# Kernel tuning notes

Measured on AMD Instinct MI355X. Metric: run time of the kernel, lower is better.

## Reference

```python
import jax, jax.numpy as jnp
import numpy as np

B, L = 64, 262144
KERNEL_SIZES = [65, 33, 17, 9]
K_LIST = [L // ks for ks in KERNEL_SIZES]  # sparsity_density per kernel


def conv1d_same(x, w):
    # x: [B, 1, L], w: [kernel_size] -> torch F.conv1d(..., padding='same')
    return jax.lax.conv_general_dilated(
        x, w[None, None, :], window_strides=(1,), padding='SAME',
        dimension_numbers=('NCH', 'OIH', 'NCH'))


def topk_absolutes_1d(x, k):
    # keep the k largest-|x| entries along the last axis, zero elsewhere
    _, idx = jax.lax.top_k(jnp.abs(x), k)          # [B, 1, k]
    kept = jnp.take_along_axis(x, idx, axis=-1)    # [B, 1, k]
    b = jnp.arange(x.shape[0])[:, None, None]
    c = jnp.arange(x.shape[1])[None, :, None]
    return jnp.zeros_like(x).at[b, c, idx].set(kept)


def setup_inputs() -> dict:
    key = jax.random.key(0)
    batch_x = jax.random.normal(key, (B, 1, L), dtype=jnp.float32)
    inp = {'batch_x': batch_x}
    for i, ks in enumerate(KERNEL_SIZES):
        inp[f'w{i}'] = 0.1 * jnp.ones((ks,), dtype=jnp.float32)
    return inp


def reference(batch_x, w0, w1, w2, w3):
    weights = [w0, w1, w2, w3]
    recon_sum = jnp.zeros_like(batch_x)
    for w, k in zip(weights, K_LIST):
        similarity = conv1d_same(batch_x, w)
        activations = topk_absolutes_1d(similarity, k)
        recon_sum = recon_sum + conv1d_same(activations, w)
    return recon_sum
```

## Files before the change

kernel.cpp:

```cpp
#include <hip/hip_runtime.h>
#include <stdint.h>


#define B_ 64
#define L_ 262144
#define NBINS 8192
#define CAPC 8192
#define LCAP 1024
#define TSUB 2304
#define SUBS 8
#define NCHUNK 15
#define XSTG 2560
#define T5 2304
#define NT5 114
#define NSCAN 16

typedef unsigned int u32;

__device__ const int d_K[4] = {4032, 7943, 15420, 29127};

__device__ __forceinline__ void k1_stage(const float* __restrict__ xr, int base,
                                         float* dst, int tid)
{
  const bool interior = (base >= 32) && (base - 32 + XSTG <= L_);
  if (interior) {
    const float* g0 = xr + (base - 32);
    const int wv = tid >> 6, lane = tid & 63;
#pragma unroll
    for (int r = 0; r < 3; ++r) {
      const int off = (r * 4 + wv) * 256;
      if (off < XSTG) {
        __builtin_amdgcn_global_load_lds(
            (const __attribute__((address_space(1))) unsigned int*)(const void*)(g0 + off + lane * 4),
            (__attribute__((address_space(3))) unsigned int*)(void*)(dst + off),
            16, 0, 0);
      }
    }
  } else {
    for (int i = tid; i < TSUB + 64; i += 256) {
      const int g = base - 32 + i;
      dst[i] = (g >= 0 && g < L_) ? xr[g] : 0.0f;
    }
  }
}

template<int KS>
__device__ __forceinline__ void k1_body(
    const float* __restrict__ xr, const float* __restrict__ w,
    float* __restrict__ yrow,
    float* xb0, float* xb1, float* yb0, float* yb1)
{
  constexpr int PAD = KS / 2;
  constexpr int OFF = 32 - PAD;
  const int tid = threadIdx.x;

  float wreg[KS];
#pragma unroll
  for (int j = 0; j < KS; ++j) wreg[j] = w[j];

  const int base0 = blockIdx.x * SUBS * TSUB;
  k1_stage(xr, base0, xb0, tid);
  __syncthreads();

  int pendBase = -1;
  float* pendBuf = nullptr;

  for (int it = 0; it < SUBS; ++it) {
    const int base = base0 + it * TSUB;
    if (base >= L_) break;
    float* xcur = (it & 1) ? xb1 : xb0;
    float* xnxt = (it & 1) ? xb0 : xb1;
    float* ycur = (it & 1) ? yb1 : yb0;
    const int nbase = base + TSUB;
    if (it + 1 < SUBS && nbase < L_)
      k1_stage(xr, nbase, xnxt, tid);

    if (pendBase >= 0) {
      const int n4 = min(TSUB, L_ - pendBase) >> 2;
      float4* dst = (float4*)(yrow + pendBase);
      for (int i = tid; i < n4; i += 256) dst[i] = ((const float4*)pendBuf)[i];
    }

    float acc[9];
#pragma unroll
    for (int r = 0; r < 9; ++r) acc[r] = 0.0f;
    const int q0 = tid * 9;
#pragma unroll
    for (int p = 0; p < KS + 8; ++p) {
      float xv = xcur[q0 + OFF + p];
#pragma unroll
      for (int r = 0; r < 9; ++r) {
        const int j = p - r;
        if (j >= 0 && j < KS) acc[r] = fmaf(xv, wreg[j], acc[r]);
      }
    }

#pragma unroll
    for (int r = 0; r < 9; ++r) ycur[q0 + r] = acc[r];
    pendBase = base; pendBuf = ycur;
    __syncthreads();
  }

  if (pendBase >= 0) {
    const int n4 = min(TSUB, L_ - pendBase) >> 2;
    float4* dst = (float4*)(yrow + pendBase);
    for (int i = tid; i < n4; i += 256) dst[i] = ((const float4*)pendBuf)[i];
  }
}

__global__ __launch_bounds__(256) void k1_conv(
    const float* __restrict__ x, const float* __restrict__ w0,
    const float* __restrict__ w1, const float* __restrict__ w2,
    const float* __restrict__ w3, float* __restrict__ y,
    int kk0, int ng)
{
  __shared__ __align__(16) float xb[2][XSTG];
  __shared__ __align__(16) float yb[2][TSUB];
  const int kg = blockIdx.y;
  const int row = blockIdx.z;
  const int rkl = row * ng + kg;
  const int kk = kk0 + kg;
  const float* xr = x + (size_t)row * L_;
  float* yrow = y + (size_t)rkl * L_;
  switch (kk) {
    case 0:  k1_body<65>(xr, w0, yrow, xb[0], xb[1], yb[0], yb[1]); break;
    case 1:  k1_body<33>(xr, w1, yrow, xb[0], xb[1], yb[0], yb[1]); break;
    case 2:  k1_body<17>(xr, w2, yrow, xb[0], xb[1], yb[0], yb[1]); break;
    default: k1_body< 9>(xr, w3, yrow, xb[0], xb[1], yb[0], yb[1]); break;
  }
}

__global__ __launch_bounds__(256) void k2_hist(
    const float* __restrict__ y, u32* __restrict__ ghist, int ng)
{
  __shared__ u32 h32[NBINS / 2];
  const int tid = threadIdx.x;
  const int rkl = blockIdx.z * ng + blockIdx.y;
  for (int i = tid; i < NBINS / 2; i += 256) h32[i] = 0u;
  __syncthreads();
  const float* yr = y + (size_t)rkl * L_;
  const int c0 = blockIdx.x * (L_ / NSCAN);
  const float4* src = (const float4*)(yr + c0);
  for (int i = tid; i < (L_ / NSCAN) / 4; i += 256) {
    float4 v = src[i];
    const float* vf = (const float*)&v;
#pragma unroll
    for (int c = 0; c < 4; ++c) {
      u32 bin = (__float_as_uint(vf[c]) & 0x7fffffffu) >> 18;
      atomicAdd(&h32[bin >> 1], 1u << (16 * (bin & 1)));
    }
  }
  __syncthreads();
  u32* gh = ghist + (size_t)rkl * NBINS;
  for (int i = tid; i < NBINS / 2; i += 256) {
    u32 v = h32[i];
    u32 lo = v & 0xffffu, hi = v >> 16;
    if (lo) atomicAdd(&gh[2 * i], lo);
    if (hi) atomicAdd(&gh[2 * i + 1], hi);
  }
}

__global__ __launch_bounds__(256) void k2_findbin(
    const u32* __restrict__ ghist, u32* __restrict__ bbin, u32* __restrict__ rrem,
    int kk0, int ng)
{
  __shared__ u32 h[NBINS];
  __shared__ u32 ssum[256];
  const int rkl = blockIdx.x;
  const u32 k = (u32)d_K[kk0 + (rkl % ng)];
  const u32* gh = ghist + (size_t)rkl * NBINS;
  for (int i = threadIdx.x; i < NBINS; i += 256) h[i] = gh[i];
  __syncthreads();
  u32 s = 0;
  for (int i = 0; i < 32; ++i) s += h[threadIdx.x * 32 + i];
  ssum[threadIdx.x] = s;
  __syncthreads();
  if (threadIdx.x == 0) {
    u32 cum = 0; int b = 0;
    for (int t = 255; t >= 0; --t) {
      if (cum + ssum[t] >= k) {
        for (int i = t * 32 + 31; i >= t * 32; --i) {
          if (cum + h[i] >= k) { b = i; break; }
          cum += h[i];
        }
        break;
      }
      cum += ssum[t];
    }
    bbin[rkl] = (u32)b;
    rrem[rkl] = k - cum;
  }
}

__global__ __launch_bounds__(256) void k3_scan(
    const float* __restrict__ y, const u32* __restrict__ bbin,
    u32* __restrict__ ccount, uint2* __restrict__ cand, int ng)
{
  __shared__ uint2 lcand[LCAP];
  __shared__ u32 lmeta[3];
  const int tid = threadIdx.x;
  const int rkl = blockIdx.z * ng + blockIdx.y;
  const u32 target = bbin[rkl];
  if (tid == 0) lmeta[0] = 0u;
  __syncthreads();
  const float* yr = y + (size_t)rkl * L_;
  const int c0 = blockIdx.x * (L_ / NSCAN);
  const float4* src = (const float4*)(yr + c0);
  for (int i = tid; i < (L_ / NSCAN) / 4; i += 256) {
    float4 v = src[i];
    const float* vf = (const float*)&v;
#pragma unroll
    for (int c = 0; c < 4; ++c) {
      u32 ab = __float_as_uint(vf[c]) & 0x7fffffffu;
      if ((ab >> 18) == target) {
        u32 slot = atomicAdd(&lmeta[0], 1u);
        if (slot < LCAP) lcand[slot] = make_uint2(ab, (u32)(c0 + 4 * i + c));
      }
    }
  }
  __syncthreads();
  if (tid == 0) {
    u32 m = lmeta[0]; if (m > LCAP) m = LCAP;
    lmeta[1] = m;
    lmeta[2] = atomicAdd(&ccount[rkl], m);
  }
  __syncthreads();
  const u32 m = lmeta[1], bse = lmeta[2];
  uint2* cd = cand + (size_t)rkl * CAPC;
  for (u32 i = tid; i < m; i += 256)
    if (bse + i < CAPC) cd[bse + i] = lcand[i];
}

__global__ __launch_bounds__(256) void k4_select(
    const uint2* __restrict__ cand, const u32* __restrict__ ccount,
    const u32* __restrict__ bbinA, const u32* __restrict__ rremA,
    u32* __restrict__ thr, u32* __restrict__ keepAll,
    u32* __restrict__ excN, u32* __restrict__ excL)
{
  __shared__ u32 cab[CAPC];
  __shared__ u32 h64[64];
  __shared__ u32 sh[3];
  __shared__ u32 lidx[64];
  __shared__ u32 lcnt;
  const int rkl = blockIdx.x;
  int n = (int)min(ccount[rkl], (u32)CAPC);
  u32 r = rremA[rkl];
  if (r > (u32)n) r = (u32)n;
  const uint2* cd = cand + (size_t)rkl * CAPC;
  for (int i = threadIdx.x; i < n; i += 256) cab[i] = cd[i].x & 0x3ffffu;

  u32 sel = 0;
  for (int round = 0; round < 3; ++round) {
    const int shift = 12 - 6 * round;
    const u32 himask = (round == 0) ? 0u : ((0x3ffffu << (shift + 6)) & 0x3ffffu);
    if (threadIdx.x < 64) h64[threadIdx.x] = 0u;
    __syncthreads();
    for (int i = threadIdx.x; i < n; i += 256) {
      u32 v = cab[i];
      if ((v & himask) == (sel & himask)) atomicAdd(&h64[(v >> shift) & 63u], 1u);
    }
    __syncthreads();
    if (threadIdx.x == 0) {
      u32 cum = 0; int d = 0;
      for (int dd = 63; dd >= 0; --dd) {
        if (cum + h64[dd] >= r) { d = dd; break; }
        cum += h64[dd];
      }
      sh[0] = (u32)d;
      sh[1] = r - cum;
      sh[2] = h64[d];
    }
    __syncthreads();
    sel |= sh[0] << shift;
    r = sh[1];
  }
  const u32 dup = sh[2];
  const u32 m = r;
  if (threadIdx.x == 0) thr[rkl] = (bbinA[rkl] << 18) | sel;

  if (m >= dup) {
    if (threadIdx.x == 0) { keepAll[rkl] = 1u; excN[rkl] = 0u; }
    return;
  }
  if (threadIdx.x == 0) lcnt = 0u;
  __syncthreads();
  for (int i = threadIdx.x; i < n; i += 256) {
    if (cab[i] == sel) {
      u32 s2 = atomicAdd(&lcnt, 1u);
      if (s2 < 64) lidx[s2] = cd[i].y;
    }
  }
  __syncthreads();
  if (threadIdx.x == 0) {
    int c = (int)min(lcnt, 64u);
    for (int i = 1; i < c; ++i) {
      u32 v = lidx[i]; int j = i - 1;
      while (j >= 0 && lidx[j] > v) { lidx[j + 1] = lidx[j]; --j; }
      lidx[j + 1] = v;
    }
    u32 mm = min(m, 32u);
    keepAll[rkl] = 0u; excN[rkl] = mm;
    for (u32 i = 0; i < mm; ++i) excL[(size_t)rkl * 32 + i] = lidx[i];
  }
}

__device__ __forceinline__ float k5_mask(float yv, int g, u32 t_ab, u32 ka,
                                         u32 en, const u32* __restrict__ excp)
{
  u32 ab = __float_as_uint(yv) & 0x7fffffffu;
  bool keep = ab > t_ab;
  if (ab == t_ab) {
    if (ka) keep = true;
    else {
      for (u32 e = 0; e < en; ++e)
        if (excp[e] == (u32)g) { keep = true; break; }
    }
  }
  return keep ? yv : 0.0f;
}

template<int KS>
__device__ __forceinline__ void k5_conv(
    const float* __restrict__ w, const float* abuf, float* accO)
{
  constexpr int PAD = KS / 2;
  constexpr int OFF2 = 32 - PAD;
  float wreg[KS];
#pragma unroll
  for (int j = 0; j < KS; ++j) wreg[j] = w[j];
  const int o0 = threadIdx.x * 9;
#pragma unroll
  for (int p = 0; p < KS + 8; ++p) {
    float av = abuf[o0 + OFF2 + p];
#pragma unroll
    for (int r = 0; r < 9; ++r) {
      const int j = p - r;
      if (j >= 0 && j < KS) accO[r] = fmaf(av, wreg[j], accO[r]);
    }
  }
}

__global__ __launch_bounds__(256) void k5_final(
    const float* __restrict__ y, const float* __restrict__ w0,
    const float* __restrict__ w1, const float* __restrict__ w2,
    const float* __restrict__ w3, const u32* __restrict__ thr,
    const u32* __restrict__ keepAll, const u32* __restrict__ excN,
    const u32* __restrict__ excL, float* __restrict__ out,
    int kk0, int ng)
{
  __shared__ __align__(16) float abuf[T5 + 64];
  const int tid = threadIdx.x;
  const int row = blockIdx.y;
  const int tile0 = blockIdx.x * T5;
  float accO[9];
#pragma unroll
  for (int r = 0; r < 9; ++r) accO[r] = 0.0f;

  for (int kg = 0; kg < ng; ++kg) {
    const int rkl = row * ng + kg;
    const int kk = kk0 + kg;
    const u32 t_ab = thr[rkl], ka = keepAll[rkl], en = excN[rkl];
    const u32* excp = excL + (size_t)rkl * 32;
    const float* yr = y + (size_t)rkl * L_;
    const bool interior = (tile0 >= 32) && (tile0 + T5 + 32 <= L_);
    if (interior) {
      const float4* src = (const float4*)(yr + tile0 - 32);
      for (int i = tid; i < (T5 + 64) / 4; i += 256) {
        float4 v = src[i];
        float* vf = (float*)&v;
#pragma unroll
        for (int c = 0; c < 4; ++c)
          vf[c] = k5_mask(vf[c], tile0 - 32 + 4 * i + c, t_ab, ka, en, excp);
        ((float4*)abuf)[i] = v;
      }
    } else {
      for (int i = tid; i < T5 + 64; i += 256) {
        int g = tile0 - 32 + i;
        float av = 0.0f;
        if (g >= 0 && g < L_) av = k5_mask(yr[g], g, t_ab, ka, en, excp);
        abuf[i] = av;
      }
    }
    __syncthreads();
    switch (kk) {
      case 0:  k5_conv<65>(w0, abuf, accO); break;
      case 1:  k5_conv<33>(w1, abuf, accO); break;
      case 2:  k5_conv<17>(w2, abuf, accO); break;
      default: k5_conv< 9>(w3, abuf, accO); break;
    }
    __syncthreads();
  }

  const int o0 = tid * 9;
#pragma unroll
  for (int r = 0; r < 9; ++r) abuf[o0 + r] = accO[r];
  __syncthreads();
  float* orow = out + (size_t)row * L_ + tile0;
  const int n4 = min(T5, L_ - tile0) / 4;
  if (kk0 == 0) {
    for (int i = tid; i < n4; i += 256)
      ((float4*)orow)[i] = ((const float4*)abuf)[i];
  } else {
    for (int i = tid; i < n4; i += 256) {
      float4 p = ((const float4*)orow)[i];
      float4 a = ((const float4*)abuf)[i];
      p.x += a.x; p.y += a.y; p.z += a.z; p.w += a.w;
      ((float4*)orow)[i] = p;
    }
  }
}

extern "C" void kernel_launch(void* const* d_in, const int* in_sizes, int n_in,
                              void* d_out, int out_size, void* d_ws, size_t ws_size,
                              hipStream_t stream)
{
  (void)in_sizes; (void)n_in; (void)out_size;
  const float* x  = (const float*)d_in[0];
  const float* w0 = (const float*)d_in[1];
  const float* w1 = (const float*)d_in[2];
  const float* w2 = (const float*)d_in[3];
  const float* w3 = (const float*)d_in[4];
  float* out = (float*)d_out;

  auto need = [](int ng) -> size_t {
    return (size_t)ng * 64 * ((size_t)L_ * 4 + NBINS * 4 + 4 * 6 + 32 * 4 + CAPC * 8);
  };
  int ng = 1;
  if (ws_size >= need(4)) ng = 4;
  else if (ws_size >= need(2)) ng = 2;

  const size_t NRK = (size_t)64 * ng;
  float* y     = (float*)d_ws;
  u32* ghist   = (u32*)(y + NRK * L_);
  u32* ccount  = ghist + NRK * NBINS;
  u32* bbin    = ccount + NRK;
  u32* rrem    = bbin + NRK;
  u32* thr     = rrem + NRK;
  u32* kAll    = thr + NRK;
  u32* excN    = kAll + NRK;
  u32* excL    = excN + NRK;
  uint2* cand  = (uint2*)(excL + NRK * 32);

  for (int kk0 = 0; kk0 < 4; kk0 += ng) {
    hipMemsetAsync(ghist, 0, (NRK * NBINS + NRK) * sizeof(u32), stream);
    dim3 g1(NCHUNK, ng, B_);
    k1_conv<<<g1, 256, 0, stream>>>(x, w0, w1, w2, w3, y, kk0, ng);
    dim3 gh(NSCAN, ng, B_);
    k2_hist<<<gh, 256, 0, stream>>>(y, ghist, ng);
    k2_findbin<<<(int)NRK, 256, 0, stream>>>(ghist, bbin, rrem, kk0, ng);
    dim3 g3(NSCAN, ng, B_);
    k3_scan<<<g3, 256, 0, stream>>>(y, bbin, ccount, cand, ng);
    k4_select<<<(int)NRK, 256, 0, stream>>>(cand, ccount, bbin, rrem, thr, kAll, excN, excL);
    dim3 g5(NT5, B_);
    k5_final<<<g5, 256, 0, stream>>>(y, w0, w1, w2, w3, thr, kAll, excN, excL, out, kk0, ng);
  }
}
```

Before: 436.4 us.

## Fuse histogram into conv kernel and coarsen bins to 4096

Builds the magnitude histogram inside the convolution kernel from register accumulators, removing the separate histogram pass that re-read the whole similarity array. The bin count is halved (shift by 19 instead of 18) so the shared histogram fits alongside the staging buffers, and the select kernel's first radix round widens to 7 bits to cover the extra low bit. ccount is now reset in findbin instead of by the memset. Coarser bins mean more candidates land in the threshold bin, which raises the risk of overflowing the local candidate capacity and adds per-element shared atomics to the conv kernel.

```diff
diff --git a/kernel.cpp b/kernel.cpp
--- a/kernel.cpp
+++ b/kernel.cpp
@@ -4,7 +4,7 @@
 
 #define B_ 64
 #define L_ 262144
-#define NBINS 8192
+#define NBINS 4096
 #define CAPC 8192
 #define LCAP 1024
 #define TSUB 2304
@@ -47,8 +47,8 @@
 template<int KS>
 __device__ __forceinline__ void k1_body(
     const float* __restrict__ xr, const float* __restrict__ w,
-    float* __restrict__ yrow,
-    float* xb0, float* xb1, float* yb0, float* yb1)
+    float* __restrict__ yrow, u32* __restrict__ gh,
+    float* xb0, float* xb1, float* yb0, float* yb1, u32* h32)
 {
   constexpr int PAD = KS / 2;
   constexpr int OFF = 32 - PAD;
@@ -57,6 +57,8 @@
   float wreg[KS];
 #pragma unroll
   for (int j = 0; j < KS; ++j) wreg[j] = w[j];
+
+  for (int i = tid; i < NBINS / 2; i += 256) h32[i] = 0u;
 
   const int base0 = blockIdx.x * SUBS * TSUB;
   k1_stage(xr, base0, xb0, tid);
@@ -97,6 +99,16 @@
 
 #pragma unroll
     for (int r = 0; r < 9; ++r) ycur[q0 + r] = acc[r];
+
+    const int g0 = base + q0;
+#pragma unroll
+    for (int r = 0; r < 9; ++r) {
+      if (g0 + r < L_) {
+        u32 bin = (__float_as_uint(acc[r]) & 0x7fffffffu) >> 19;
+        atomicAdd(&h32[bin >> 1], 1u << (16 * (bin & 1)));
+      }
+    }
+
     pendBase = base; pendBuf = ycur;
     __syncthreads();
   }
@@ -106,37 +118,83 @@
     float4* dst = (float4*)(yrow + pendBase);
     for (int i = tid; i < n4; i += 256) dst[i] = ((const float4*)pendBuf)[i];
   }
+
+  for (int i = tid; i < NBINS / 2; i += 256) {
+    u32 v = h32[i];
+    u32 lo = v & 0xffffu, hi = v >> 16;
+    if (lo) atomicAdd(&gh[2 * i], lo);
+    if (hi) atomicAdd(&gh[2 * i + 1], hi);
+  }
 }
 
 __global__ __launch_bounds__(256) void k1_conv(
     const float* __restrict__ x, const float* __restrict__ w0,
     const float* __restrict__ w1, const float* __restrict__ w2,
     const float* __restrict__ w3, float* __restrict__ y,
-    int kk0, int ng)
+    u32* __restrict__ ghist, int kk0, int ng)
 {
   __shared__ __align__(16) float xb[2][XSTG];
   __shared__ __align__(16) float yb[2][TSUB];
+  __shared__ u32 h32[NBINS / 2];
   const int kg = blockIdx.y;
   const int row = blockIdx.z;
   const int rkl = row * ng + kg;
   const int kk = kk0 + kg;
   const float* xr = x + (size_t)row * L_;
   float* yrow = y + (size_t)rkl * L_;
+  u32* gh = ghist + (size_t)rkl * NBINS;
   switch (kk) {
-    case 0:  k1_body<65>(xr, w0, yrow, xb[0], xb[1], yb[0], yb[1]); break;
-    case 1:  k1_body<33>(xr, w1, yrow, xb[0], xb[1], yb[0], yb[1]); break;
-    case 2:  k1_body<17>(xr, w2, yrow, xb[0], xb[1], yb[0], yb[1]); break;
-    default: k1_body< 9>(xr, w3, yrow, xb[0], xb[1], yb[0], yb[1]); break;
-  }
-}
-
-__global__ __launch_bounds__(256) void k2_hist(
-    const float* __restrict__ y, u32* __restrict__ ghist, int ng)
-{
-  __shared__ u32 h32[NBINS / 2];
+    case 0:  k1_body<65>(xr, w0, yrow, gh, xb[0], xb[1], yb[0], yb[1], h32); break;
+    case 1:  k1_body<33>(xr, w1, yrow, gh, xb[0], xb[1], yb[0], yb[1], h32); break;
+    case 2:  k1_body<17>(xr, w2, yrow, gh, xb[0], xb[1], yb[0], yb[1], h32); break;
+    default: k1_body< 9>(xr, w3, yrow, gh, xb[0], xb[1], yb[0], yb[1], h32); break;
+  }
+}
+
+__global__ __launch_bounds__(256) void k2_findbin(
+    const u32* __restrict__ ghist, u32* __restrict__ bbin, u32* __restrict__ rrem,
+    u32* __restrict__ ccount, int kk0, int ng)
+{
+  __shared__ u32 h[NBINS];
+  __shared__ u32 ssum[256];
+  const int tid = threadIdx.x;
+  const int rkl = blockIdx.x;
+  const u32 k = (u32)d_K[kk0 + (rkl % ng)];
+  const u32* gh = ghist + (size_t)rkl * NBINS;
+  for (int i = tid; i < NBINS; i += 256) h[i] = gh[i];
+  __syncthreads();
+  u32 s = 0;
+  for (int i = 0; i < 16; ++i) s += h[tid * 16 + i];
+  ssum[tid] = s;
+  __syncthreads();
+  if (tid == 0) {
+    u32 cum = 0; int b = 0;
+    for (int t = 255; t >= 0; --t) {
+      if (cum + ssum[t] >= k) {
+        for (int i = t * 16 + 15; i >= t * 16; --i) {
+          if (cum + h[i] >= k) { b = i; break; }
+          cum += h[i];
+        }
+        break;
+      }
+      cum += ssum[t];
+    }
+    bbin[rkl] = (u32)b;
+    rrem[rkl] = k - cum;
+    ccount[rkl] = 0u;
+  }
+}
+
+__global__ __launch_bounds__(256) void k3_scan(
+    const float* __restrict__ y, const u32* __restrict__ bbin,
+    u32* __restrict__ ccount, uint2* __restrict__ cand, int ng)
+{
+  __shared__ uint2 lcand[LCAP];
+  __shared__ u32 lmeta[3];
   const int tid = threadIdx.x;
   const int rkl = blockIdx.z * ng + blockIdx.y;
-  for (int i = tid; i < NBINS / 2; i += 256) h32[i] = 0u;
+  const u32 target = bbin[rkl];
+  if (tid == 0) lmeta[0] = 0u;
   __syncthreads();
   const float* yr = y + (size_t)rkl * L_;
   const int c0 = blockIdx.x * (L_ / NSCAN);
@@ -146,73 +204,8 @@
     const float* vf = (const float*)&v;
 #pragma unroll
     for (int c = 0; c < 4; ++c) {
-      u32 bin = (__float_as_uint(vf[c]) & 0x7fffffffu) >> 18;
-      atomicAdd(&h32[bin >> 1], 1u << (16 * (bin & 1)));
-    }
-  }
-  __syncthreads();
-  u32* gh = ghist + (size_t)rkl * NBINS;
-  for (int i = tid; i < NBINS / 2; i += 256) {
-    u32 v = h32[i];
-    u32 lo = v & 0xffffu, hi = v >> 16;
-    if (lo) atomicAdd(&gh[2 * i], lo);
-    if (hi) atomicAdd(&gh[2 * i + 1], hi);
-  }
-}
-
-__global__ __launch_bounds__(256) void k2_findbin(
-    const u32* __restrict__ ghist, u32* __restrict__ bbin, u32* __restrict__ rrem,
-    int kk0, int ng)
-{
-  __shared__ u32 h[NBINS];
-  __shared__ u32 ssum[256];
-  const int rkl = blockIdx.x;
-  const u32 k = (u32)d_K[kk0 + (rkl % ng)];
-  const u32* gh = ghist + (size_t)rkl * NBINS;
-  for (int i = threadIdx.x; i < NBINS; i += 256) h[i] = gh[i];
-  __syncthreads();
-  u32 s = 0;
-  for (int i = 0; i < 32; ++i) s += h[threadIdx.x * 32 + i];
-  ssum[threadIdx.x] = s;
-  __syncthreads();
-  if (threadIdx.x == 0) {
-    u32 cum = 0; int b = 0;
-    for (int t = 255; t >= 0; --t) {
-      if (cum + ssum[t] >= k) {
-        for (int i = t * 32 + 31; i >= t * 32; --i) {
-          if (cum + h[i] >= k) { b = i; break; }
-          cum += h[i];
-        }
-        break;
-      }
-      cum += ssum[t];
-    }
-    bbin[rkl] = (u32)b;
-    rrem[rkl] = k - cum;
-  }
-}
-
-__global__ __launch_bounds__(256) void k3_scan(
-    const float* __restrict__ y, const u32* __restrict__ bbin,
-    u32* __restrict__ ccount, uint2* __restrict__ cand, int ng)
-{
-  __shared__ uint2 lcand[LCAP];
-  __shared__ u32 lmeta[3];
-  const int tid = threadIdx.x;
-  const int rkl = blockIdx.z * ng + blockIdx.y;
-  const u32 target = bbin[rkl];
-  if (tid == 0) lmeta[0] = 0u;
-  __syncthreads();
-  const float* yr = y + (size_t)rkl * L_;
-  const int c0 = blockIdx.x * (L_ / NSCAN);
-  const float4* src = (const float4*)(yr + c0);
-  for (int i = tid; i < (L_ / NSCAN) / 4; i += 256) {
-    float4 v = src[i];
-    const float* vf = (const float*)&v;
-#pragma unroll
-    for (int c = 0; c < 4; ++c) {
       u32 ab = __float_as_uint(vf[c]) & 0x7fffffffu;
-      if ((ab >> 18) == target) {
+      if ((ab >> 19) == target) {
         u32 slot = atomicAdd(&lmeta[0], 1u);
         if (slot < LCAP) lcand[slot] = make_uint2(ab, (u32)(c0 + 4 * i + c));
       }
@@ -238,7 +231,7 @@
     u32* __restrict__ excN, u32* __restrict__ excL)
 {
   __shared__ u32 cab[CAPC];
-  __shared__ u32 h64[64];
+  __shared__ u32 h128[128];
   __shared__ u32 sh[3];
   __shared__ u32 lidx[64];
   __shared__ u32 lcnt;
@@ -247,28 +240,32 @@
   u32 r = rremA[rkl];
   if (r > (u32)n) r = (u32)n;
   const uint2* cd = cand + (size_t)rkl * CAPC;
-  for (int i = threadIdx.x; i < n; i += 256) cab[i] = cd[i].x & 0x3ffffu;
+  for (int i = threadIdx.x; i < n; i += 256) cab[i] = cd[i].x & 0x7ffffu;
 
   u32 sel = 0;
+#pragma unroll
   for (int round = 0; round < 3; ++round) {
-    const int shift = 12 - 6 * round;
-    const u32 himask = (round == 0) ? 0u : ((0x3ffffu << (shift + 6)) & 0x3ffffu);
-    if (threadIdx.x < 64) h64[threadIdx.x] = 0u;
+    const int shift = (round == 0) ? 12 : (round == 1) ? 6 : 0;
+    const int width = (round == 0) ? 7 : 6;
+    const int hb = shift + width;
+    const int nb = 1 << width;
+    if (threadIdx.x < nb) h128[threadIdx.x] = 0u;
     __syncthreads();
     for (int i = threadIdx.x; i < n; i += 256) {
       u32 v = cab[i];
-      if ((v & himask) == (sel & himask)) atomicAdd(&h64[(v >> shift) & 63u], 1u);
+      if ((v >> hb) == (sel >> hb))
+        atomicAdd(&h128[(v >> shift) & (u32)(nb - 1)], 1u);
     }
     __syncthreads();
     if (threadIdx.x == 0) {
       u32 cum = 0; int d = 0;
-      for (int dd = 63; dd >= 0; --dd) {
-        if (cum + h64[dd] >= r) { d = dd; break; }
-        cum += h64[dd];
+      for (int dd = nb - 1; dd >= 0; --dd) {
+        if (cum + h128[dd] >= r) { d = dd; break; }
+        cum += h128[dd];
       }
       sh[0] = (u32)d;
       sh[1] = r - cum;
-      sh[2] = h64[d];
+      sh[2] = h128[d];
     }
     __syncthreads();
     sel |= sh[0] << shift;
@@ -276,7 +273,7 @@
   }
   const u32 dup = sh[2];
   const u32 m = r;
-  if (threadIdx.x == 0) thr[rkl] = (bbinA[rkl] << 18) | sel;
+  if (threadIdx.x == 0) thr[rkl] = (bbinA[rkl] << 19) | sel;
 
   if (m >= dup) {
     if (threadIdx.x == 0) { keepAll[rkl] = 1u; excN[rkl] = 0u; }
@@ -423,7 +420,7 @@
   float* out = (float*)d_out;
 
   auto need = [](int ng) -> size_t {
-    return (size_t)ng * 64 * ((size_t)L_ * 4 + NBINS * 4 + 4 * 6 + 32 * 4 + CAPC * 8);
+    return (size_t)ng * 64 * ((size_t)L_ * 4 + NBINS * 4 + 6 * 4 + 32 * 4 + CAPC * 8);
   };
   int ng = 1;
   if (ws_size >= need(4)) ng = 4;
@@ -442,12 +439,10 @@
   uint2* cand  = (uint2*)(excL + NRK * 32);
 
   for (int kk0 = 0; kk0 < 4; kk0 += ng) {
-    hipMemsetAsync(ghist, 0, (NRK * NBINS + NRK) * sizeof(u32), stream);
+    hipMemsetAsync(ghist, 0, NRK * NBINS * sizeof(u32), stream);
     dim3 g1(NCHUNK, ng, B_);
-    k1_conv<<<g1, 256, 0, stream>>>(x, w0, w1, w2, w3, y, kk0, ng);
-    dim3 gh(NSCAN, ng, B_);
-    k2_hist<<<gh, 256, 0, stream>>>(y, ghist, ng);
-    k2_findbin<<<(int)NRK, 256, 0, stream>>>(ghist, bbin, rrem, kk0, ng);
+    k1_conv<<<g1, 256, 0, stream>>>(x, w0, w1, w2, w3, y, ghist, kk0, ng);
+    k2_findbin<<<(int)NRK, 256, 0, stream>>>(ghist, bbin, rrem, ccount, kk0, ng);
     dim3 g3(NSCAN, ng, B_);
     k3_scan<<<g3, 256, 0, stream>>>(y, bbin, ccount, cand, ng);
     k4_select<<<(int)NRK, 256, 0, stream>>>(cand, ccount, bbin, rrem, thr, kAll, excN, excL);
```

After: 426.2 us. -2.3%, faster.
